# Performance work log

Hardware: AMD Instinct MI355X
Metric: run time of the kernel (lower is better)

The kernel has to match this reference:

```python
import jax, jax.numpy as jnp
import numpy as np

N, E, F, T, H = 100000, 3_200_000, 64, 12, 32


def _lin(k, fin, fout):
    s = 1.0 / np.sqrt(fin)
    k1, k2 = jax.random.split(k)
    W = jax.random.uniform(k1, (fin, fout), jnp.float32, -s, s)
    b = jax.random.uniform(k2, (fout,), jnp.float32, -s, s)
    return W, b


def _lstm_w(k, fin):
    s = 1.0 / np.sqrt(H)
    k1, k2, k3, k4 = jax.random.split(k, 4)
    return (jax.random.uniform(k1, (4 * H, fin), jnp.float32, -s, s),
            jax.random.uniform(k2, (4 * H, H), jnp.float32, -s, s),
            jax.random.uniform(k3, (4 * H,), jnp.float32, -s, s),
            jax.random.uniform(k4, (4 * H,), jnp.float32, -s, s))


def setup_inputs() -> dict:
    key = jax.random.key(0)
    ks = jax.random.split(key, 12)
    x = jax.random.normal(ks[0], (N, F), jnp.float32)
    edge_index = jax.random.randint(ks[1], (2, E), 0, N, dtype=jnp.int32)
    W_fp, b_fp = _lin(ks[2], F, 64)
    W_g1, b_g1 = _lin(ks[3], 64, 64)
    W_g2, b_g2 = _lin(ks[4], 64, 32)
    W_g3, b_g3 = _lin(ks[5], 32, 16)
    W_tp, b_tp = _lin(ks[6], 1, 16)
    Wih0, Whh0, bih0, bhh0 = _lstm_w(ks[7], 16)
    Wih1, Whh1, bih1, bhh1 = _lstm_w(ks[8], H)
    W_fc1, b_fc1 = _lin(ks[9], H, 16)
    W_fc2, b_fc2 = _lin(ks[10], 16, 1)
    return dict(x=x, edge_index=edge_index, W_fp=W_fp, b_fp=b_fp,
                W_g1=W_g1, b_g1=b_g1, W_g2=W_g2, b_g2=b_g2, W_g3=W_g3, b_g3=b_g3,
                W_tp=W_tp, b_tp=b_tp,
                Wih0=Wih0, Whh0=Whh0, bih0=bih0, bhh0=bhh0,
                Wih1=Wih1, Whh1=Whh1, bih1=bih1, bhh1=bhh1,
                W_fc1=W_fc1, b_fc1=b_fc1, W_fc2=W_fc2, b_fc2=b_fc2)


def reference(x, edge_index, W_fp, b_fp, W_g1, b_g1, W_g2, b_g2, W_g3, b_g3,
              W_tp, b_tp, Wih0, Whh0, bih0, bhh0, Wih1, Whh1, bih1, bhh1,
              W_fc1, b_fc1, W_fc2, b_fc2):
    n = x.shape[0]
    loops = jnp.arange(n, dtype=edge_index.dtype)
    src = jnp.concatenate([edge_index[0], loops])  # self-loops, PyG GCNConv default
    dst = jnp.concatenate([edge_index[1], loops])
    deg = jax.ops.segment_sum(jnp.ones_like(src, dtype=x.dtype), dst, num_segments=n)
    dis = deg ** -0.5  # deg >= 1 because of self-loops
    norm = dis[src] * dis[dst]  # [E+N]

    def gcn(h, W, b):
        h = h @ W  # transform then propagate (PyG order)
        agg = jax.ops.segment_sum(h[src] * norm[:, None], dst, num_segments=n)
        return agg + b

    h = jax.nn.relu(x @ W_fp + b_fp)
    h = jax.nn.relu(gcn(h, W_g1, b_g1))        # dropout inactive (eval mode)
    h = jax.nn.relu(gcn(h, W_g2, b_g2))
    h_gcn = jax.nn.relu(gcn(h, W_g3, b_g3))    # NOTE: overwritten in original forward (dead)

    # temporal branch: last T raw features -> [N, T, 1] -> proj to 16
    t = x[:, -T:].reshape(n, T, 1) @ W_tp + b_tp  # [N, T, 16]

    def step(carry, xt):
        h0, c0, h1, c1 = carry
        g = xt @ Wih0.T + h0 @ Whh0.T + (bih0 + bhh0)
        i, f, gg, o = jnp.split(g, 4, axis=-1)  # torch gate order i,f,g,o
        c0 = jax.nn.sigmoid(f) * c0 + jax.nn.sigmoid(i) * jnp.tanh(gg)
        h0 = jax.nn.sigmoid(o) * jnp.tanh(c0)
        g = h0 @ Wih1.T + h1 @ Whh1.T + (bih1 + bhh1)
        i, f, gg, o = jnp.split(g, 4, axis=-1)
        c1 = jax.nn.sigmoid(f) * c1 + jax.nn.sigmoid(i) * jnp.tanh(gg)
        h1 = jax.nn.sigmoid(o) * jnp.tanh(c1)
        return (h0, c0, h1, c1), None

    z = jnp.zeros((n, H), x.dtype)
    (h0, c0, h1, c1), _ = jax.lax.scan(step, (z, z, z, z), jnp.swapaxes(t, 0, 1))
    out = jax.nn.relu(h1 @ W_fc1 + b_fc1) @ W_fc2 + b_fc2  # [N, 1]
    return out
```

## Files before the change

### kernel.cpp

```cpp
#include <hip/hip_runtime.h>


#define TSTEPS 12
#define BS 256
#define NPB 128

__device__ __forceinline__ float fsig(float x) {
    float e = __expf(-x);
    return __builtin_amdgcn_rcpf(1.0f + e);
}

__device__ __forceinline__ float ftanh(float x) {
    float ax = fabsf(x);
    float e = __expf(-2.0f * ax);
    float r = (1.0f - e) * __builtin_amdgcn_rcpf(1.0f + e);
    return x < 0.0f ? -r : r;
}

__global__ void precomp_kernel(const float* __restrict__ Wih0,
                               const float* __restrict__ Wtp,
                               const float* __restrict__ btp,
                               const float* __restrict__ bih0,
                               const float* __restrict__ bhh0,
                               const float* __restrict__ bih1,
                               const float* __restrict__ bhh1,
                               float* __restrict__ ws) {
    int r = threadIdx.x;
    if (r < 128) {
        float a = 0.0f, c = 0.0f;
#pragma unroll
        for (int k = 0; k < 16; ++k) {
            float w = Wih0[r * 16 + k];
            a += w * Wtp[k];
            c += w * btp[k];
        }
        const int g4 = r >> 5;
        const int j  = r & 31;
        ws[j * 8 + g4]       = a;
        ws[j * 8 + 4 + g4]   = c + bih0[r] + bhh0[r];
        ws[256 + j * 4 + g4] = bih1[r] + bhh1[r];
    }
}

__device__ __forceinline__ float dot8(const float4 a0, const float4 a1,
                                      const float h[8]) {
    return a0.x*h[0] + a0.y*h[1] + a0.z*h[2] + a0.w*h[3]
         + a1.x*h[4] + a1.y*h[5] + a1.z*h[6] + a1.w*h[7];
}

__device__ __forceinline__ float rs4(float v0, float v1, float v2, float v3,
                                     bool hi2, bool hi1) {
    float sa = hi2 ? v0 : v2;
    float ka = hi2 ? v2 : v0;
    float sb = hi2 ? v1 : v3;
    float kb = hi2 ? v3 : v1;
    float u0 = ka + __shfl_xor(sa, 2);
    float u1 = kb + __shfl_xor(sb, 2);
    float sc = hi1 ? u0 : u1;
    float kc = hi1 ? u1 : u0;
    return kc + __shfl_xor(sc, 1);
}

__global__ __launch_bounds__(BS) void lstm_kernel(
    const float* __restrict__ x,
    const float* __restrict__ Whh0,
    const float* __restrict__ Wih1,
    const float* __restrict__ Whh1,
    const float* __restrict__ Wfc1,
    const float* __restrict__ bfc1,
    const float* __restrict__ Wfc2,
    const float* __restrict__ bfc2,
    const float* __restrict__ pre,
    float* __restrict__ out, int N)
{
    __shared__ __align__(16) float sW[12288];
    __shared__ float sc0[16 * BS];
    __shared__ float sc1[16 * BS];

    const int tid = threadIdx.x;
#pragma unroll
    for (int i = 0; i < 16; ++i) sW[i * BS + tid]        = Whh0[i * BS + tid];
#pragma unroll
    for (int i = 0; i < 16; ++i) sW[4096 + i * BS + tid] = Wih1[i * BS + tid];
#pragma unroll
    for (int i = 0; i < 16; ++i) sW[8192 + i * BS + tid] = Whh1[i * BS + tid];
#pragma unroll
    for (int jj = 0; jj < 8; ++jj) {
        sc0[jj * BS + tid] = 0.0f;  sc0[2048 + jj * BS + tid] = 0.0f;
        sc1[jj * BS + tid] = 0.0f;  sc1[2048 + jj * BS + tid] = 0.0f;
    }
    __syncthreads();

    const int s    = tid & 3;
    const int slot = tid >> 2;
    const int so8  = s * 8;
    const bool hi2 = (s & 2) != 0;
    const bool hi1 = (s & 1) != 0;
    const int nA = blockIdx.x * NPB + slot;
    const int nB = nA + 64;
    const int nnA = (nA < N) ? nA : (N > 0 ? N - 1 : 0);
    const int nnB = (nB < N) ? nB : (N > 0 ? N - 1 : 0);
    const float* xrA = x + (size_t)nnA * 64 + 52;
    const float* xrB = x + (size_t)nnB * 64 + 52;

    float h0A[8], h0B[8], h1A[8], h1B[8], hnA[8], hnB[8];
#pragma unroll
    for (int k = 0; k < 8; ++k) { h0A[k] = 0.0f; h0B[k] = 0.0f; h1A[k] = 0.0f; h1B[k] = 0.0f; }

#pragma unroll 1
    for (int t = 0; t < TSTEPS; ++t) {
        const float xvA = xrA[t];
        const float xvB = xrB[t];

#pragma unroll
        for (int jj = 0; jj < 8; ++jj) {
            const int jown = so8 + jj;
            float SA[4], SB[4];
#pragma unroll
            for (int gate = 0; gate < 4; ++gate) {
                float4 w0[4], w1[4];
#pragma unroll
                for (int g = 0; g < 4; ++g) {
                    const float* w = &sW[(gate * 32 + g * 8 + jj) * 32 + so8];
                    w0[g] = ((const float4*)w)[0];
                    w1[g] = ((const float4*)w)[1];
                }
                float pA[4], pB[4];
#pragma unroll
                for (int g = 0; g < 4; ++g) {
                    pA[g] = dot8(w0[g], w1[g], h0A);
                    pB[g] = dot8(w0[g], w1[g], h0B);
                }
                SA[gate] = rs4(pA[0], pA[1], pA[2], pA[3], hi2, hi1);
                SB[gate] = rs4(pB[0], pB[1], pB[2], pB[3], hi2, hi1);
                __builtin_amdgcn_sched_barrier(0);
            }
            const float4 pAq = ((const float4*)pre)[jown * 2];
            const float4 pCq = ((const float4*)pre)[jown * 2 + 1];
            {
                const float gi = SA[0] + pCq.x + xvA * pAq.x;
                const float gf = SA[1] + pCq.y + xvA * pAq.y;
                const float gG = SA[2] + pCq.z + xvA * pAq.z;
                const float go = SA[3] + pCq.w + xvA * pAq.w;
                const int ci = jj * BS + tid;
                const float cc = fsig(gf) * sc0[ci] + fsig(gi) * ftanh(gG);
                sc0[ci] = cc;
                hnA[jj] = fsig(go) * ftanh(cc);
            }
            {
                const float gi = SB[0] + pCq.x + xvB * pAq.x;
                const float gf = SB[1] + pCq.y + xvB * pAq.y;
                const float gG = SB[2] + pCq.z + xvB * pAq.z;
                const float go = SB[3] + pCq.w + xvB * pAq.w;
                const int ci = 2048 + jj * BS + tid;
                const float cc = fsig(gf) * sc0[ci] + fsig(gi) * ftanh(gG);
                sc0[ci] = cc;
                hnB[jj] = fsig(go) * ftanh(cc);
            }
        }
#pragma unroll
        for (int k = 0; k < 8; ++k) { h0A[k] = hnA[k]; h0B[k] = hnB[k]; }

#pragma unroll
        for (int jj = 0; jj < 8; ++jj) {
            const int jown = so8 + jj;
            float SA[4], SB[4];
#pragma unroll
            for (int gate = 0; gate < 4; ++gate) {
                float pA[4], pB[4];
                {
                    float4 w0[4], w1[4];
#pragma unroll
                    for (int g = 0; g < 4; ++g) {
                        const float* w = &sW[4096 + (gate * 32 + g * 8 + jj) * 32 + so8];
                        w0[g] = ((const float4*)w)[0];
                        w1[g] = ((const float4*)w)[1];
                    }
#pragma unroll
                    for (int g = 0; g < 4; ++g) {
                        pA[g] = dot8(w0[g], w1[g], h0A);
                        pB[g] = dot8(w0[g], w1[g], h0B);
                    }
                }
                __builtin_amdgcn_sched_barrier(0);
                {
                    float4 w0[4], w1[4];
#pragma unroll
                    for (int g = 0; g < 4; ++g) {
                        const float* w = &sW[8192 + (gate * 32 + g * 8 + jj) * 32 + so8];
                        w0[g] = ((const float4*)w)[0];
                        w1[g] = ((const float4*)w)[1];
                    }
#pragma unroll
                    for (int g = 0; g < 4; ++g) {
                        pA[g] += dot8(w0[g], w1[g], h1A);
                        pB[g] += dot8(w0[g], w1[g], h1B);
                    }
                }
                SA[gate] = rs4(pA[0], pA[1], pA[2], pA[3], hi2, hi1);
                SB[gate] = rs4(pB[0], pB[1], pB[2], pB[3], hi2, hi1);
                __builtin_amdgcn_sched_barrier(0);
            }
            const float4 pD = ((const float4*)(pre + 256))[jown];
            {
                const float gi = SA[0] + pD.x;
                const float gf = SA[1] + pD.y;
                const float gG = SA[2] + pD.z;
                const float go = SA[3] + pD.w;
                const int ci = jj * BS + tid;
                const float cc = fsig(gf) * sc1[ci] + fsig(gi) * ftanh(gG);
                sc1[ci] = cc;
                hnA[jj] = fsig(go) * ftanh(cc);
            }
            {
                const float gi = SB[0] + pD.x;
                const float gf = SB[1] + pD.y;
                const float gG = SB[2] + pD.z;
                const float go = SB[3] + pD.w;
                const int ci = 2048 + jj * BS + tid;
                const float cc = fsig(gf) * sc1[ci] + fsig(gi) * ftanh(gG);
                sc1[ci] = cc;
                hnB[jj] = fsig(go) * ftanh(cc);
            }
        }
#pragma unroll
        for (int k = 0; k < 8; ++k) { h1A[k] = hnA[k]; h1B[k] = hnB[k]; }
    }

    {
        float am[16];
#pragma unroll
        for (int m = 0; m < 16; ++m) am[m] = 0.0f;
#pragma unroll 1
        for (int kk = 0; kk < 8; ++kk) {
            const float* row = Wfc1 + (size_t)(so8 + kk) * 16;
            const float4 r0 = ((const float4*)row)[0];
            const float4 r1 = ((const float4*)row)[1];
            const float4 r2 = ((const float4*)row)[2];
            const float4 r3 = ((const float4*)row)[3];
            const float hv = h1A[kk];
            am[ 0] += r0.x*hv; am[ 1] += r0.y*hv; am[ 2] += r0.z*hv; am[ 3] += r0.w*hv;
            am[ 4] += r1.x*hv; am[ 5] += r1.y*hv; am[ 6] += r1.z*hv; am[ 7] += r1.w*hv;
            am[ 8] += r2.x*hv; am[ 9] += r2.y*hv; am[10] += r2.z*hv; am[11] += r2.w*hv;
            am[12] += r3.x*hv; am[13] += r3.y*hv; am[14] += r3.z*hv; am[15] += r3.w*hv;
        }
        float acc = bfc2[0];
#pragma unroll
        for (int m = 0; m < 16; ++m) {
            float a = am[m];
            a += __shfl_xor(a, 1); a += __shfl_xor(a, 2);
            acc += fmaxf(a + bfc1[m], 0.0f) * Wfc2[m];
        }
        if (s == 0 && nA < N) out[nA] = acc;
    }
    {
        float am[16];
#pragma unroll
        for (int m = 0; m < 16; ++m) am[m] = 0.0f;
#pragma unroll 1
        for (int kk = 0; kk < 8; ++kk) {
            const float* row = Wfc1 + (size_t)(so8 + kk) * 16;
            const float4 r0 = ((const float4*)row)[0];
            const float4 r1 = ((const float4*)row)[1];
            const float4 r2 = ((const float4*)row)[2];
            const float4 r3 = ((const float4*)row)[3];
            const float hv = h1B[kk];
            am[ 0] += r0.x*hv; am[ 1] += r0.y*hv; am[ 2] += r0.z*hv; am[ 3] += r0.w*hv;
            am[ 4] += r1.x*hv; am[ 5] += r1.y*hv; am[ 6] += r1.z*hv; am[ 7] += r1.w*hv;
            am[ 8] += r2.x*hv; am[ 9] += r2.y*hv; am[10] += r2.z*hv; am[11] += r2.w*hv;
            am[12] += r3.x*hv; am[13] += r3.y*hv; am[14] += r3.z*hv; am[15] += r3.w*hv;
        }
        float acc = bfc2[0];
#pragma unroll
        for (int m = 0; m < 16; ++m) {
            float a = am[m];
            a += __shfl_xor(a, 1); a += __shfl_xor(a, 2);
            acc += fmaxf(a + bfc1[m], 0.0f) * Wfc2[m];
        }
        if (s == 0 && nB < N) out[nB] = acc;
    }
}

extern "C" void kernel_launch(void* const* d_in, const int* in_sizes, int n_in,
                              void* d_out, int out_size, void* d_ws, size_t ws_size,
                              hipStream_t stream) {
    (void)n_in; (void)out_size; (void)ws_size;
    const float* x    = (const float*)d_in[0];
    const float* Wtp  = (const float*)d_in[10];
    const float* btp  = (const float*)d_in[11];
    const float* Wih0 = (const float*)d_in[12];
    const float* Whh0 = (const float*)d_in[13];
    const float* bih0 = (const float*)d_in[14];
    const float* bhh0 = (const float*)d_in[15];
    const float* Wih1 = (const float*)d_in[16];
    const float* Whh1 = (const float*)d_in[17];
    const float* bih1 = (const float*)d_in[18];
    const float* bhh1 = (const float*)d_in[19];
    const float* Wfc1 = (const float*)d_in[20];
    const float* bfc1 = (const float*)d_in[21];
    const float* Wfc2 = (const float*)d_in[22];
    const float* bfc2 = (const float*)d_in[23];

    float* out = (float*)d_out;
    float* pre = (float*)d_ws;

    const int N = in_sizes[0] / 64;

    precomp_kernel<<<1, 128, 0, stream>>>(Wih0, Wtp, btp, bih0, bhh0, bih1, bhh1, pre);
    lstm_kernel<<<(N + NPB - 1) / NPB, BS, 0, stream>>>(
        x, Whh0, Wih1, Whh1, Wfc1, bfc1, Wfc2, bfc2, pre, out, N);
}
```

Measured before the change: 1.407 ms.

## Split each LSTM node across 8 lanes and keep cell state in registers

Each node is now handled by 8 threads instead of 4, each owning 4 hidden units, and the block grows from 256 to 512 threads. The dot products shrink to 4-wide and the reduction becomes an 8-way shuffle butterfly. The cell states move from shared-memory arrays into registers, which removes per-step LDS traffic and frees shared memory. The cost is more shuffle work per gate and a different occupancy and register tradeoff.

```diff
diff --git a/kernel.cpp b/kernel.cpp
--- a/kernel.cpp
+++ b/kernel.cpp
@@ -2,7 +2,7 @@
 
 
 #define TSTEPS 12
-#define BS 256
+#define BS 512
 #define NPB 128
 
 __device__ __forceinline__ float fsig(float x) {
@@ -42,23 +42,23 @@
     }
 }
 
-__device__ __forceinline__ float dot8(const float4 a0, const float4 a1,
-                                      const float h[8]) {
-    return a0.x*h[0] + a0.y*h[1] + a0.z*h[2] + a0.w*h[3]
-         + a1.x*h[4] + a1.y*h[5] + a1.z*h[6] + a1.w*h[7];
-}
-
-__device__ __forceinline__ float rs4(float v0, float v1, float v2, float v3,
-                                     bool hi2, bool hi1) {
-    float sa = hi2 ? v0 : v2;
-    float ka = hi2 ? v2 : v0;
-    float sb = hi2 ? v1 : v3;
-    float kb = hi2 ? v3 : v1;
-    float u0 = ka + __shfl_xor(sa, 2);
-    float u1 = kb + __shfl_xor(sb, 2);
-    float sc = hi1 ? u0 : u1;
-    float kc = hi1 ? u1 : u0;
-    return kc + __shfl_xor(sc, 1);
+__device__ __forceinline__ float dot4(const float4 w, const float h[4]) {
+    return w.x*h[0] + w.y*h[1] + w.z*h[2] + w.w*h[3];
+}
+
+__device__ __forceinline__ float rs8(const float p[8],
+                                     bool b4, bool b2, bool b1) {
+    float k0 = b4 ? p[4] : p[0], s0 = b4 ? p[0] : p[4];
+    float k1 = b4 ? p[5] : p[1], s1 = b4 ? p[1] : p[5];
+    float k2 = b4 ? p[6] : p[2], s2 = b4 ? p[2] : p[6];
+    float k3 = b4 ? p[7] : p[3], s3 = b4 ? p[3] : p[7];
+    k0 += __shfl_xor(s0, 4); k1 += __shfl_xor(s1, 4);
+    k2 += __shfl_xor(s2, 4); k3 += __shfl_xor(s3, 4);
+    float m0 = b2 ? k2 : k0, t0 = b2 ? k0 : k2;
+    float m1 = b2 ? k3 : k1, t1 = b2 ? k1 : k3;
+    m0 += __shfl_xor(t0, 2); m1 += __shfl_xor(t1, 2);
+    float r = b1 ? m1 : m0,  q = b1 ? m0 : m1;
+    return r + __shfl_xor(q, 1);
 }
 
 __global__ __launch_bounds__(BS) void lstm_kernel(
@@ -74,28 +74,20 @@
     float* __restrict__ out, int N)
 {
     __shared__ __align__(16) float sW[12288];
-    __shared__ float sc0[16 * BS];
-    __shared__ float sc1[16 * BS];
 
     const int tid = threadIdx.x;
 #pragma unroll
-    for (int i = 0; i < 16; ++i) sW[i * BS + tid]        = Whh0[i * BS + tid];
-#pragma unroll
-    for (int i = 0; i < 16; ++i) sW[4096 + i * BS + tid] = Wih1[i * BS + tid];
-#pragma unroll
-    for (int i = 0; i < 16; ++i) sW[8192 + i * BS + tid] = Whh1[i * BS + tid];
-#pragma unroll
-    for (int jj = 0; jj < 8; ++jj) {
-        sc0[jj * BS + tid] = 0.0f;  sc0[2048 + jj * BS + tid] = 0.0f;
-        sc1[jj * BS + tid] = 0.0f;  sc1[2048 + jj * BS + tid] = 0.0f;
-    }
+    for (int i = 0; i < 8; ++i) sW[i * BS + tid]        = Whh0[i * BS + tid];
+#pragma unroll
+    for (int i = 0; i < 8; ++i) sW[4096 + i * BS + tid] = Wih1[i * BS + tid];
+#pragma unroll
+    for (int i = 0; i < 8; ++i) sW[8192 + i * BS + tid] = Whh1[i * BS + tid];
     __syncthreads();
 
-    const int s    = tid & 3;
-    const int slot = tid >> 2;
-    const int so8  = s * 8;
-    const bool hi2 = (s & 2) != 0;
-    const bool hi1 = (s & 1) != 0;
+    const int u    = tid & 7;
+    const int slot = tid >> 3;
+    const int so4  = u * 4;
+    const bool b4 = (u & 4) != 0, b2 = (u & 2) != 0, b1 = (u & 1) != 0;
     const int nA = blockIdx.x * NPB + slot;
     const int nB = nA + 64;
     const int nnA = (nA < N) ? nA : (N > 0 ? N - 1 : 0);
@@ -103,9 +95,14 @@
     const float* xrA = x + (size_t)nnA * 64 + 52;
     const float* xrB = x + (size_t)nnB * 64 + 52;
 
-    float h0A[8], h0B[8], h1A[8], h1B[8], hnA[8], hnB[8];
-#pragma unroll
-    for (int k = 0; k < 8; ++k) { h0A[k] = 0.0f; h0B[k] = 0.0f; h1A[k] = 0.0f; h1B[k] = 0.0f; }
+    float h0A[4], h0B[4], h1A[4], h1B[4];
+    float c0A[4], c0B[4], c1A[4], c1B[4];
+    float hnA[4], hnB[4];
+#pragma unroll
+    for (int k = 0; k < 4; ++k) {
+        h0A[k] = 0.0f; h0B[k] = 0.0f; h1A[k] = 0.0f; h1B[k] = 0.0f;
+        c0A[k] = 0.0f; c0B[k] = 0.0f; c1A[k] = 0.0f; c1B[k] = 0.0f;
+    }
 
 #pragma unroll 1
     for (int t = 0; t < TSTEPS; ++t) {
@@ -113,28 +110,25 @@
         const float xvB = xrB[t];
 
 #pragma unroll
-        for (int jj = 0; jj < 8; ++jj) {
-            const int jown = so8 + jj;
+        for (int jj = 0; jj < 4; ++jj) {
             float SA[4], SB[4];
 #pragma unroll
             for (int gate = 0; gate < 4; ++gate) {
-                float4 w0[4], w1[4];
-#pragma unroll
-                for (int g = 0; g < 4; ++g) {
-                    const float* w = &sW[(gate * 32 + g * 8 + jj) * 32 + so8];
-                    w0[g] = ((const float4*)w)[0];
-                    w1[g] = ((const float4*)w)[1];
+                float4 w[8];
+#pragma unroll
+                for (int g = 0; g < 8; ++g)
+                    w[g] = *(const float4*)&sW[(gate * 32 + g * 4 + jj) * 32 + so4];
+                float pA[8], pB[8];
+#pragma unroll
+                for (int g = 0; g < 8; ++g) {
+                    pA[g] = dot4(w[g], h0A);
+                    pB[g] = dot4(w[g], h0B);
                 }
-                float pA[4], pB[4];
-#pragma unroll
-                for (int g = 0; g < 4; ++g) {
-                    pA[g] = dot8(w0[g], w1[g], h0A);
-                    pB[g] = dot8(w0[g], w1[g], h0B);
-                }
-                SA[gate] = rs4(pA[0], pA[1], pA[2], pA[3], hi2, hi1);
-                SB[gate] = rs4(pB[0], pB[1], pB[2], pB[3], hi2, hi1);
+                SA[gate] = rs8(pA, b4, b2, b1);
+                SB[gate] = rs8(pB, b4, b2, b1);
                 __builtin_amdgcn_sched_barrier(0);
             }
+            const int jown = so4 + jj;
             const float4 pAq = ((const float4*)pre)[jown * 2];
             const float4 pCq = ((const float4*)pre)[jown * 2 + 1];
             {
@@ -142,9 +136,8 @@
                 const float gf = SA[1] + pCq.y + xvA * pAq.y;
                 const float gG = SA[2] + pCq.z + xvA * pAq.z;
                 const float go = SA[3] + pCq.w + xvA * pAq.w;
-                const int ci = jj * BS + tid;
-                const float cc = fsig(gf) * sc0[ci] + fsig(gi) * ftanh(gG);
-                sc0[ci] = cc;
+                const float cc = fsig(gf) * c0A[jj] + fsig(gi) * ftanh(gG);
+                c0A[jj] = cc;
                 hnA[jj] = fsig(go) * ftanh(cc);
             }
             {
@@ -152,64 +145,56 @@
                 const float gf = SB[1] + pCq.y + xvB * pAq.y;
                 const float gG = SB[2] + pCq.z + xvB * pAq.z;
                 const float go = SB[3] + pCq.w + xvB * pAq.w;
-                const int ci = 2048 + jj * BS + tid;
-                const float cc = fsig(gf) * sc0[ci] + fsig(gi) * ftanh(gG);
-                sc0[ci] = cc;
+                const float cc = fsig(gf) * c0B[jj] + fsig(gi) * ftanh(gG);
+                c0B[jj] = cc;
                 hnB[jj] = fsig(go) * ftanh(cc);
             }
         }
 #pragma unroll
-        for (int k = 0; k < 8; ++k) { h0A[k] = hnA[k]; h0B[k] = hnB[k]; }
-
-#pragma unroll
-        for (int jj = 0; jj < 8; ++jj) {
-            const int jown = so8 + jj;
+        for (int k = 0; k < 4; ++k) { h0A[k] = hnA[k]; h0B[k] = hnB[k]; }
+
+#pragma unroll
+        for (int jj = 0; jj < 4; ++jj) {
             float SA[4], SB[4];
 #pragma unroll
             for (int gate = 0; gate < 4; ++gate) {
-                float pA[4], pB[4];
+                float pA[8], pB[8];
                 {
-                    float4 w0[4], w1[4];
-#pragma unroll
-                    for (int g = 0; g < 4; ++g) {
-                        const float* w = &sW[4096 + (gate * 32 + g * 8 + jj) * 32 + so8];
-                        w0[g] = ((const float4*)w)[0];
-                        w1[g] = ((const float4*)w)[1];
-                    }
-#pragma unroll
-                    for (int g = 0; g < 4; ++g) {
-                        pA[g] = dot8(w0[g], w1[g], h0A);
-                        pB[g] = dot8(w0[g], w1[g], h0B);
+                    float4 w[8];
+#pragma unroll
+                    for (int g = 0; g < 8; ++g)
+                        w[g] = *(const float4*)&sW[4096 + (gate * 32 + g * 4 + jj) * 32 + so4];
+#pragma unroll
+                    for (int g = 0; g < 8; ++g) {
+                        pA[g] = dot4(w[g], h0A);
+                        pB[g] = dot4(w[g], h0B);
                     }
                 }
                 __builtin_amdgcn_sched_barrier(0);
                 {
-                    float4 w0[4], w1[4];
-#pragma unroll
-                    for (int g = 0; g < 4; ++g) {
-                        const float* w = &sW[8192 + (gate * 32 + g * 8 + jj) * 32 + so8];
-                        w0[g] = ((const float4*)w)[0];
-                        w1[g] = ((const float4*)w)[1];
-                    }
-#pragma unroll
-                    for (int g = 0; g < 4; ++g) {
-                        pA[g] += dot8(w0[g], w1[g], h1A);
-                        pB[g] += dot8(w0[g], w1[g], h1B);
+                    float4 w[8];
+#pragma unroll
+                    for (int g = 0; g < 8; ++g)
+                        w[g] = *(const float4*)&sW[8192 + (gate * 32 + g * 4 + jj) * 32 + so4];
+#pragma unroll
+                    for (int g = 0; g < 8; ++g) {
+                        pA[g] += dot4(w[g], h1A);
+                        pB[g] += dot4(w[g], h1B);
                     }
                 }
-                SA[gate] = rs4(pA[0], pA[1], pA[2], pA[3], hi2, hi1);
-                SB[gate] = rs4(pB[0], pB[1], pB[2], pB[3], hi2, hi1);
+                SA[gate] = rs8(pA, b4, b2, b1);
+                SB[gate] = rs8(pB, b4, b2, b1);
                 __builtin_amdgcn_sched_barrier(0);
             }
+            const int jown = so4 + jj;
             const float4 pD = ((const float4*)(pre + 256))[jown];
             {
                 const float gi = SA[0] + pD.x;
                 const float gf = SA[1] + pD.y;
                 const float gG = SA[2] + pD.z;
                 const float go = SA[3] + pD.w;
-                const int ci = jj * BS + tid;
-                const float cc = fsig(gf) * sc1[ci] + fsig(gi) * ftanh(gG);
-                sc1[ci] = cc;
+                const float cc = fsig(gf) * c1A[jj] + fsig(gi) * ftanh(gG);
+                c1A[jj] = cc;
                 hnA[jj] = fsig(go) * ftanh(cc);
             }
             {
@@ -217,14 +202,13 @@
                 const float gf = SB[1] + pD.y;
                 const float gG = SB[2] + pD.z;
                 const float go = SB[3] + pD.w;
-                const int ci = 2048 + jj * BS + tid;
-                const float cc = fsig(gf) * sc1[ci] + fsig(gi) * ftanh(gG);
-                sc1[ci] = cc;
+                const float cc = fsig(gf) * c1B[jj] + fsig(gi) * ftanh(gG);
+                c1B[jj] = cc;
                 hnB[jj] = fsig(go) * ftanh(cc);
             }
         }
 #pragma unroll
-        for (int k = 0; k < 8; ++k) { h1A[k] = hnA[k]; h1B[k] = hnB[k]; }
+        for (int k = 0; k < 4; ++k) { h1A[k] = hnA[k]; h1B[k] = hnB[k]; }
     }
 
     {
@@ -232,8 +216,8 @@
 #pragma unroll
         for (int m = 0; m < 16; ++m) am[m] = 0.0f;
 #pragma unroll 1
-        for (int kk = 0; kk < 8; ++kk) {
-            const float* row = Wfc1 + (size_t)(so8 + kk) * 16;
+        for (int kk = 0; kk < 4; ++kk) {
+            const float* row = Wfc1 + (size_t)(so4 + kk) * 16;
             const float4 r0 = ((const float4*)row)[0];
             const float4 r1 = ((const float4*)row)[1];
             const float4 r2 = ((const float4*)row)[2];
@@ -248,18 +232,18 @@
 #pragma unroll
         for (int m = 0; m < 16; ++m) {
             float a = am[m];
-            a += __shfl_xor(a, 1); a += __shfl_xor(a, 2);
+            a += __shfl_xor(a, 1); a += __shfl_xor(a, 2); a += __shfl_xor(a, 4);
             acc += fmaxf(a + bfc1[m], 0.0f) * Wfc2[m];
         }
-        if (s == 0 && nA < N) out[nA] = acc;
+        if (u == 0 && nA < N) out[nA] = acc;
     }
     {
         float am[16];
 #pragma unroll
         for (int m = 0; m < 16; ++m) am[m] = 0.0f;
 #pragma unroll 1
-        for (int kk = 0; kk < 8; ++kk) {
-            const float* row = Wfc1 + (size_t)(so8 + kk) * 16;
+        for (int kk = 0; kk < 4; ++kk) {
+            const float* row = Wfc1 + (size_t)(so4 + kk) * 16;
             const float4 r0 = ((const float4*)row)[0];
             const float4 r1 = ((const float4*)row)[1];
             const float4 r2 = ((const float4*)row)[2];
@@ -274,10 +258,10 @@
 #pragma unroll
         for (int m = 0; m < 16; ++m) {
             float a = am[m];
-            a += __shfl_xor(a, 1); a += __shfl_xor(a, 2);
+            a += __shfl_xor(a, 1); a += __shfl_xor(a, 2); a += __shfl_xor(a, 4);
             acc += fmaxf(a + bfc1[m], 0.0f) * Wfc2[m];
         }
-        if (s == 0 && nB < N) out[nB] = acc;
+        if (u == 0 && nB < N) out[nB] = acc;
     }
 }
 
```

Measured after the change: 2.881 ms. +104.7%, slower.
